# Kernel tuning notes

Measured on AMD Instinct MI355X. Metric: run time of the kernel, lower is better.

Reference implementation:

```python
import jax, jax.numpy as jnp
import numpy as np

SELECTED_CLASS = 1  # matches init_kwargs


def _edt_sq(mask):
    """Exact squared Euclidean distance of each pixel to the nearest False pixel.
    Matches scipy.ndimage.distance_transform_edt(mask)**2 (2-pass separable,
    column scan + exact row-wise parabola minimization done brute-force in chunks).
    mask: (H, W) bool.
    """
    H, W = mask.shape
    BIG = np.float32(H + W)  # > any possible true distance, safe sentinel
    g = np.where(mask, BIG, np.float32(0.0)).astype(np.float32)
    for i in range(1, H):
        np.minimum(g[i], g[i - 1] + 1, out=g[i])
    for i in range(H - 2, -1, -1):
        np.minimum(g[i], g[i + 1] + 1, out=g[i])
    g2 = g * g  # (H, W) squared column distances
    k = np.arange(W, dtype=np.float32)
    d2 = np.empty((H, W), np.float32)
    CH = 64  # chunk of output columns to bound temp memory
    for j0 in range(0, W, CH):
        j = k[j0:j0 + CH]
        diff2 = (j[None, :] - k[:, None]) ** 2  # (W, Jc)
        d2[:, j0:j0 + CH] = (g2[:, :, None] + diff2[None]).min(axis=1)
    return d2


def _inner_boundary(mask):
    """skimage.segmentation.find_boundaries(mask, mode='inner'), connectivity=1:
    foreground pixels with at least one in-image 4-neighbor in background."""
    p = np.pad(mask, 1, constant_values=True)
    ero = p[1:-1, :-2] & p[1:-1, 2:] & p[:-2, 1:-1] & p[2:, 1:-1] & mask
    return mask & ~ero


def compute_sdf_np(y_true_sel):
    """Normalized signed distance map, faithful to BoundaryLoss.compute_sdf.
    y_true_sel: (B, 1, H, W) float; returns (B, 1, H, W) float32 in [-1, 1]."""
    masks = y_true_sel[:, 0].astype(bool)
    B, H, W = masks.shape
    out = np.zeros((B, 1, H, W), np.float32)
    for b in range(B):
        m = masks[b]
        if not m.any():
            continue  # original leaves zeros
        posdis = np.sqrt(_edt_sq(m))
        negdis = np.sqrt(_edt_sq(~m))
        sdf = (negdis - negdis.min()) / (negdis.max() - negdis.min()) \
            - (posdis - posdis.min()) / (posdis.max() - posdis.min())
        sdf[_inner_boundary(m)] = 0.0
        out[b, 0] = sdf
    return out


def setup_inputs():
    key = jax.random.key(0)
    k1, k2 = jax.random.split(key)
    B, C, H, W = 8, 4, 512, 512
    y_pred = jax.random.normal(k1, (B, C, H, W), dtype=jnp.float32)
    y_true = jax.random.randint(k2, (B, C, H, W), 0, 2).astype(jnp.float32)
    return {"y_pred": y_pred, "y_true": y_true}


def reference(y_pred, y_true):
    sel = SELECTED_CLASS
    # GT signed distance map (host-side, non-differentiable, as in the original
    # which round-trips through scipy on CPU): shape (B, 1, H, W)
    gt_sdf = jnp.asarray(compute_sdf_np(np.asarray(y_true[:, sel:sel + 1])))
    pc = jax.nn.sigmoid(y_pred)  # (B, C, H, W)
    # torch.einsum('bchw,bchw->bchw', pc, dc) with dc having c=1 broadcasts over C
    mult = pc * gt_sdf
    return mult.mean(axis=(1, 2, 3)).mean()
```

## Files before the change

### kernel.cpp

```cpp
#include <hip/hip_runtime.h>
#include <math.h>

#define B 8
#define C 4
#define H 512
#define W 512
#define SEL 1
#define BIGI 1024
#define NPIX (B*H*W)
#define CH 64
#define RC 8
#define TC 32
#define NSEG 16
#define LL 4
#define CINF 3000
#define G 4
#define NRU (B*H/G)

__global__ __launch_bounds__(512) void col_two_level(const float* __restrict__ ytrue,
                                                     unsigned short* __restrict__ gpkT,
                                                     unsigned* __restrict__ sumsD,
                                                     unsigned* __restrict__ sumsU) {
    __shared__ int sP[NSEG][TC + 1], sN[NSEG][TC + 1];
    __shared__ int sCP[NSEG][TC + 1], sCN[NSEG][TC + 1];

    int blk = blockIdx.x;
    int b   = blk >> 7;
    int rem = blk & 127;
    int jt  = rem >> 3;
    int rc  = rem & 7;
    int tid = threadIdx.x;
    int tx  = tid & (TC - 1);
    int ty  = tid >> 5;
    int j   = jt * TC + tx;
    int i0  = rc * CH + ty * LL;

    const float* m = ytrue + ((size_t)b * C + SEL) * H * W + j;
    int gfp[LL], gfn[LL];
    int pp = BIGI, pn = BIGI;
    #pragma unroll
    for (int r = 0; r < LL; ++r) {
        bool fg = (m[(size_t)(i0 + r) * W] != 0.0f);
        int vp = fg ? BIGI : 0;
        int vn = fg ? 0 : BIGI;
        vp = min(vp, pp + 1); gfp[r] = vp; pp = vp;
        vn = min(vn, pn + 1); gfn[r] = vn; pn = vn;
    }
    sP[ty][tx] = pp - ty * LL;
    sN[ty][tx] = pn - ty * LL;
    __syncthreads();

    int col = tid >> 4, seg = tid & 15;
    int wp = sP[seg][col], wn = sN[seg][col];
    #pragma unroll
    for (int d = 1; d < NSEG; d <<= 1) {
        int a1 = __shfl_up(wp, d, 16);
        int a2 = __shfl_up(wn, d, 16);
        if (seg >= d) { wp = min(wp, a1); wn = min(wn, a2); }
    }
    if (seg < NSEG - 1) {
        sCP[seg + 1][col] = seg * LL + wp;
        sCN[seg + 1][col] = seg * LL + wn;
    } else {
        int jj = jt * TC + col;
        sumsD[((size_t)(b * RC + rc)) * W + jj] =
            (unsigned)(seg * LL + wp) | ((unsigned)(seg * LL + wn) << 16);
    }
    if (seg == 0) { sCP[0][col] = BIGI; sCN[0][col] = BIGI; }
    __syncthreads();

    int cp = sCP[ty][tx], cn = sCN[ty][tx];
    int lbp = 1 << 20, lbn = 1 << 20;
    #pragma unroll
    for (int r = 0; r < LL; ++r) {
        int vp = min(gfp[r], cp + 1 + r); gfp[r] = vp; lbp = min(lbp, vp + r);
        int vn = min(gfn[r], cn + 1 + r); gfn[r] = vn; lbn = min(lbn, vn + r);
    }
    sP[ty][tx] = lbp + ty * LL;
    sN[ty][tx] = lbn + ty * LL;
    __syncthreads();

    int w2p = sP[seg][col], w2n = sN[seg][col];
    #pragma unroll
    for (int d = 1; d < NSEG; d <<= 1) {
        int a1 = __shfl_down(w2p, d, 16);
        int a2 = __shfl_down(w2n, d, 16);
        if (seg + d < NSEG) { w2p = min(w2p, a1); w2n = min(w2n, a2); }
    }
    if (seg > 0) {
        sCP[seg - 1][col] = w2p - seg * LL;
        sCN[seg - 1][col] = w2n - seg * LL;
    } else {
        int jj = jt * TC + col;
        sumsU[((size_t)(b * RC + rc)) * W + jj] =
            (unsigned)w2p | ((unsigned)w2n << 16);
    }
    if (seg == NSEG - 1) { sCP[NSEG - 1][col] = BIGI; sCN[NSEG - 1][col] = BIGI; }
    __syncthreads();

    int pbp = sCP[ty][tx], pbn = sCN[ty][tx];
    unsigned short g4[LL];
    #pragma unroll
    for (int r = LL - 1; r >= 0; --r) {
        int vp = min(gfp[r], pbp + 1); pbp = vp;
        int vn = min(gfn[r], pbn + 1); pbn = vn;
        int fg = (vn == 0) ? 1 : 0;
        int g2 = vp + vn;
        g4[r] = (unsigned short)((g2 << 1) | fg);
    }
    ushort4 pk; pk.x = g4[0]; pk.y = g4[1]; pk.z = g4[2]; pk.w = g4[3];
    *(ushort4*)(gpkT + (((size_t)b * (H / 4) + (i0 >> 2)) * W + j) * 4) = pk;
}

__global__ __launch_bounds__(512) void row_fused(const unsigned short* __restrict__ gpkT,
                                                 const unsigned* __restrict__ sumsD,
                                                 const unsigned* __restrict__ sumsU,
                                                 const float* __restrict__ ypred,
                                                 float* __restrict__ rowpart) {
    __shared__ float s1[G][W];
    __shared__ float sw[4][8];

    int blk = blockIdx.x;
    int b = blk >> 7;
    int g = blk & 127;
    int i0 = g * G;
    int rc = i0 >> 6;
    int j = threadIdx.x;

    const unsigned* sd = sumsD + (size_t)b * RC * W + j;
    const unsigned* su = sumsU + (size_t)b * RC * W + j;
    int Ap = CINF, An = CINF, Bp = CINF, Bn = CINF;
    #pragma unroll
    for (int q = 0; q < RC; ++q) {
        if (q < rc) {
            unsigned dv = sd[(size_t)q * W];
            int e = q * CH + CH - 1;
            Ap = min(Ap, (int)(dv & 0xFFFFu) - e);
            An = min(An, (int)(dv >> 16) - e);
        } else if (q > rc) {
            unsigned uv = su[(size_t)q * W];
            int s0 = q * CH;
            Bp = min(Bp, (int)(uv & 0xFFFFu) + s0);
            Bn = min(Bn, (int)(uv >> 16) + s0);
        }
    }

    const ushort4 v4 = *(const ushort4*)(gpkT + (((size_t)b * (H / 4) + g) * W + j) * 4);
    unsigned short vv[4] = { v4.x, v4.y, v4.z, v4.w };
    float svr[G];
    #pragma unroll
    for (int r = 0; r < G; ++r) {
        int ii = i0 + r;
        unsigned v = vv[r];
        int fg = v & 1;
        int gv = v >> 1;
        int gp = fg ? gv : 0;
        int gn = fg ? 0 : gv;
        gp = min(gp, min(Ap + ii, Bp - ii));
        gn = min(gn, min(An + ii, Bn - ii));
        int gg = gp + gn;
        float sv = (float)(gg * gg);
        sv = fg ? sv : -sv;
        svr[r] = sv;
        s1[r][j] = sv;
    }
    __syncthreads();

    int jl1 = (j >= 1) ? j - 1 : j, jr1 = (j < W - 1) ? j + 1 : j;
    int jl2 = (j >= 2) ? j - 2 : j, jr2 = (j < W - 2) ? j + 2 : j;

    float mxp = 0.f, mxn = 0.f, A = 0.f, Bv = 0.f;
    #pragma unroll
    for (int r = 0; r < G; ++r) {
        float sv = svr[r];
        bool fg = (sv > 0.f);
        float sgn = fg ? 1.f : -1.f;
        float bq = fabsf(sv);
        float u1 = s1[r][jl1], u2 = s1[r][jr1], u3 = s1[r][jl2], u4 = s1[r][jr2];
        bq = fminf(bq, fmaxf(u1 * sgn, 0.f) + 1.f);
        bq = fminf(bq, fmaxf(u2 * sgn, 0.f) + 1.f);
        bq = fminf(bq, fmaxf(u3 * sgn, 0.f) + 4.f);
        bq = fminf(bq, fmaxf(u4 * sgn, 0.f) + 4.f);
        float r2 = 9.f, drr = 7.f;
        for (int rr = 3; rr < W; ++rr) {
            if (r2 >= bq) break;
            int jl = j - rr, jr = j + rr;
            if (jl >= 0) { float u = s1[r][jl]; bq = fminf(bq, fmaxf(u * sgn, 0.f) + r2); }
            if (jr < W)  { float u = s1[r][jr]; bq = fminf(bq, fmaxf(u * sgn, 0.f) + r2); }
            r2 += drr; drr += 2.f;
        }
        float d = sqrtf(bq);
        bool bnd = fg && (bq == 1.0f);

        const float* yp = ypred + ((size_t)b * C * H + i0 + r) * W + j;
        float s = 0.f;
        #pragma unroll
        for (int cc = 0; cc < C; ++cc) {
            float x = yp[(size_t)cc * H * W];
            s += 1.0f / (1.0f + __expf(-x));
        }
        float se = bnd ? 0.f : s;
        mxp = fmaxf(mxp, fg ? bq : 0.f);
        mxn = fmaxf(mxn, fg ? 0.f : bq);
        A  += fg ? se * d : 0.f;
        Bv += fg ? 0.f : se * d;
    }

    for (int off = 32; off >= 1; off >>= 1) {
        mxp = fmaxf(mxp, __shfl_down(mxp, off));
        mxn = fmaxf(mxn, __shfl_down(mxn, off));
        A  += __shfl_down(A, off);
        Bv += __shfl_down(Bv, off);
    }
    int wave = threadIdx.x >> 6, lane = threadIdx.x & 63;
    if (lane == 0) { sw[0][wave] = mxp; sw[1][wave] = mxn; sw[2][wave] = A; sw[3][wave] = Bv; }
    __syncthreads();
    if (threadIdx.x == 0) {
        float a0 = sw[0][0], a1 = sw[1][0], a2 = sw[2][0], a3 = sw[3][0];
        #pragma unroll
        for (int w = 1; w < 8; ++w) {
            a0 = fmaxf(a0, sw[0][w]); a1 = fmaxf(a1, sw[1][w]);
            a2 += sw[2][w]; a3 += sw[3][w];
        }
        *(float4*)(rowpart + (size_t)blk * 4) = make_float4(a0, a1, a2, a3);
    }
}

__global__ __launch_bounds__(512) void batch_final(const float* __restrict__ rowpart,
                                                   float* __restrict__ out) {
    __shared__ double sacc[8];
    int bw = threadIdx.x >> 6;
    int lane = threadIdx.x & 63;
    const float4* rv = (const float4*)(rowpart + (size_t)bw * 128 * 4);
    float4 e0 = rv[lane];
    float4 e1 = rv[lane + 64];
    float mxp = fmaxf(e0.x, e1.x), mxn = fmaxf(e0.y, e1.y);
    float A = e0.z + e1.z, Bv = e0.w + e1.w;
    for (int off = 32; off >= 1; off >>= 1) {
        mxp = fmaxf(mxp, __shfl_down(mxp, off));
        mxn = fmaxf(mxn, __shfl_down(mxn, off));
        A  += __shfl_down(A, off);
        Bv += __shfl_down(Bv, off);
    }
    if (lane == 0) {
        float pmax = sqrtf(mxp), nmax = sqrtf(mxn);
        float invp = (pmax > 0.f) ? 1.0f / pmax : 0.0f;
        float invn = (nmax > 0.f) ? 1.0f / nmax : 0.0f;
        sacc[bw] = (pmax > 0.f) ? (double)(invn * Bv - invp * A) : 0.0;
    }
    __syncthreads();
    if (threadIdx.x == 0) {
        double tt = 0.0;
        #pragma unroll
        for (int q = 0; q < 8; ++q) tt += sacc[q];
        out[0] = (float)(tt / (double)((size_t)B * C * H * W));
    }
}

extern "C" void kernel_launch(void* const* d_in, const int* in_sizes, int n_in,
                              void* d_out, int out_size, void* d_ws, size_t ws_size,
                              hipStream_t stream) {
    const float* ypred = (const float*)d_in[0];
    const float* ytrue = (const float*)d_in[1];
    float* out = (float*)d_out;

    unsigned short* gpkT = (unsigned short*)d_ws;
    unsigned* sumsD = (unsigned*)(gpkT + NPIX);
    unsigned* sumsU = sumsD + (size_t)B * RC * W;
    float* rowpart = (float*)(sumsU + (size_t)B * RC * W);

    col_two_level<<<B * 16 * RC, 512, 0, stream>>>(ytrue, gpkT, sumsD, sumsU);
    row_fused<<<NRU, 512, 0, stream>>>(gpkT, sumsD, sumsU, ypred, rowpart);
    batch_final<<<1, 512, 0, stream>>>(rowpart, out);
}
```

Baseline: 24.61 us.

## Process eight rows per row block, prefetch y_pred, use fast sigmoid intrinsics

Each row_fused block now handles 8 rows instead of 4, halving the block count, and batch_final is adjusted to read 64 partials per batch. All y_pred values are loaded into registers before the barrier so their latency overlaps the shared-memory fill. The sigmoid uses native exp2 and rcp builtins and the sqrt uses the native intrinsic, trading a little precision for fewer instructions. Larger per-thread state raises register pressure and leaves fewer blocks to fill the GPU.

```diff
diff --git a/kernel.cpp b/kernel.cpp
--- a/kernel.cpp
+++ b/kernel.cpp
@@ -14,8 +14,9 @@
 #define NSEG 16
 #define LL 4
 #define CINF 3000
-#define G 4
+#define G 8
 #define NRU (B*H/G)
+#define LOG2E 1.4426950408889634f
 
 __global__ __launch_bounds__(512) void col_two_level(const float* __restrict__ ytrue,
                                                      unsigned short* __restrict__ gpkT,
@@ -121,8 +122,8 @@
     __shared__ float sw[4][8];
 
     int blk = blockIdx.x;
-    int b = blk >> 7;
-    int g = blk & 127;
+    int b = blk >> 6;
+    int g = blk & 63;
     int i0 = g * G;
     int rc = i0 >> 6;
     int j = threadIdx.x;
@@ -145,24 +146,35 @@
         }
     }
 
-    const ushort4 v4 = *(const ushort4*)(gpkT + (((size_t)b * (H / 4) + g) * W + j) * 4);
-    unsigned short vv[4] = { v4.x, v4.y, v4.z, v4.w };
     float svr[G];
     #pragma unroll
+    for (int h = 0; h < G; h += 4) {
+        const ushort4 v4 = *(const ushort4*)(gpkT + (((size_t)b * (H / 4) + ((i0 + h) >> 2)) * W + j) * 4);
+        unsigned short vv[4] = { v4.x, v4.y, v4.z, v4.w };
+        #pragma unroll
+        for (int r = 0; r < 4; ++r) {
+            int ii = i0 + h + r;
+            unsigned v = vv[r];
+            int fg = v & 1;
+            int gv = v >> 1;
+            int gp = fg ? gv : 0;
+            int gn = fg ? 0 : gv;
+            gp = min(gp, min(Ap + ii, Bp - ii));
+            gn = min(gn, min(An + ii, Bn - ii));
+            int gg = gp + gn;
+            float sv = (float)(gg * gg);
+            sv = fg ? sv : -sv;
+            svr[h + r] = sv;
+            s1[h + r][j] = sv;
+        }
+    }
+
+    float yv[G][C];
+    #pragma unroll
     for (int r = 0; r < G; ++r) {
-        int ii = i0 + r;
-        unsigned v = vv[r];
-        int fg = v & 1;
-        int gv = v >> 1;
-        int gp = fg ? gv : 0;
-        int gn = fg ? 0 : gv;
-        gp = min(gp, min(Ap + ii, Bp - ii));
-        gn = min(gn, min(An + ii, Bn - ii));
-        int gg = gp + gn;
-        float sv = (float)(gg * gg);
-        sv = fg ? sv : -sv;
-        svr[r] = sv;
-        s1[r][j] = sv;
+        const float* yp = ypred + ((size_t)b * C * H + i0 + r) * W + j;
+        #pragma unroll
+        for (int cc = 0; cc < C; ++cc) yv[r][cc] = yp[(size_t)cc * H * W];
     }
     __syncthreads();
 
@@ -189,16 +201,13 @@
             if (jr < W)  { float u = s1[r][jr]; bq = fminf(bq, fmaxf(u * sgn, 0.f) + r2); }
             r2 += drr; drr += 2.f;
         }
-        float d = sqrtf(bq);
+        float d = __builtin_amdgcn_sqrtf(bq);
         bool bnd = fg && (bq == 1.0f);
 
-        const float* yp = ypred + ((size_t)b * C * H + i0 + r) * W + j;
-        float s = 0.f;
-        #pragma unroll
-        for (int cc = 0; cc < C; ++cc) {
-            float x = yp[(size_t)cc * H * W];
-            s += 1.0f / (1.0f + __expf(-x));
-        }
+        float s = __builtin_amdgcn_rcpf(1.0f + __builtin_amdgcn_exp2f(-yv[r][0] * LOG2E))
+                + __builtin_amdgcn_rcpf(1.0f + __builtin_amdgcn_exp2f(-yv[r][1] * LOG2E))
+                + __builtin_amdgcn_rcpf(1.0f + __builtin_amdgcn_exp2f(-yv[r][2] * LOG2E))
+                + __builtin_amdgcn_rcpf(1.0f + __builtin_amdgcn_exp2f(-yv[r][3] * LOG2E));
         float se = bnd ? 0.f : s;
         mxp = fmaxf(mxp, fg ? bq : 0.f);
         mxn = fmaxf(mxn, fg ? 0.f : bq);
@@ -231,11 +240,10 @@
     __shared__ double sacc[8];
     int bw = threadIdx.x >> 6;
     int lane = threadIdx.x & 63;
-    const float4* rv = (const float4*)(rowpart + (size_t)bw * 128 * 4);
+    const float4* rv = (const float4*)(rowpart + (size_t)bw * 64 * 4);
     float4 e0 = rv[lane];
-    float4 e1 = rv[lane + 64];
-    float mxp = fmaxf(e0.x, e1.x), mxn = fmaxf(e0.y, e1.y);
-    float A = e0.z + e1.z, Bv = e0.w + e1.w;
+    float mxp = e0.x, mxn = e0.y;
+    float A = e0.z, Bv = e0.w;
     for (int off = 32; off >= 1; off >>= 1) {
         mxp = fmaxf(mxp, __shfl_down(mxp, off));
         mxn = fmaxf(mxn, __shfl_down(mxn, off));
```

After: 24.19 us, median of 2. Within noise of the previous version (-1.7%).
